# Optimization experiments

Measured on AMD Instinct MI355X. Metric: run time of the kernel, lower is better.

The kernel has to match this reference:

```python
import jax, jax.numpy as jnp
import numpy as np

EPS = 1e-5
K = 9
DILATION = 1

def bn(x, g, b, m, v):
    # x: (B,C,N,1), inference-mode BatchNorm2d with running stats
    sh = (1, -1, 1, 1)
    return (x - m.reshape(sh)) * (g.reshape(sh) / jnp.sqrt(v.reshape(sh) + EPS)) + b.reshape(sh)

def conv1x1(x, w, b):
    # w: (Cout, Cin), x: (B,Cin,N,1)
    return jnp.einsum('oc,bcnj->bonj', w, x) + b.reshape(1, -1, 1, 1)

def knn_idx(feat, k):
    # feat: (B,C,N) -> (B,N,k) indices of k nearest nodes (incl. self)
    xt = jnp.transpose(feat, (0, 2, 1))  # (B,N,C)
    x2 = jnp.sum(xt * xt, axis=-1)       # (B,N)
    dist = x2[:, :, None] - 2.0 * jnp.einsum('bnc,bmc->bnm', xt, xt) + x2[:, None, :]
    _, idx = jax.lax.top_k(-dist, k)
    return idx

def setup_inputs():
    key = jax.random.key(0)
    ks = jax.random.split(key, 24)
    B, C, H, W = 16, 256, 32, 32
    HID = 512
    def g(i, shape, s=1.0):
        return jax.random.normal(ks[i], shape, dtype=jnp.float32) * s
    def pos(i, shape):
        return jax.random.uniform(ks[i], shape, dtype=jnp.float32, minval=0.5, maxval=1.5)
    return {
        'x': g(0, (B, C, H, W)),
        'fc1_w': g(1, (C, C), 0.05), 'fc1_b': g(2, (C,), 0.05),
        'bn1_g': pos(3, (C,)), 'bn1_b': g(4, (C,), 0.1), 'bn1_m': g(5, (C,), 0.1), 'bn1_v': pos(6, (C,)),
        'gc_w': g(7, (HID, 2 * C), 0.05), 'gc_b': g(8, (HID,), 0.05),
        'gbn_g': pos(9, (HID,)), 'gbn_b': g(10, (HID,), 0.1), 'gbn_m': g(11, (HID,), 0.1), 'gbn_v': pos(12, (HID,)),
        'bn2_g': pos(13, (HID,)), 'bn2_b': g(14, (HID,), 0.1), 'bn2_m': g(15, (HID,), 0.1), 'bn2_v': pos(16, (HID,)),
        'fc2_w': g(17, (C, HID), 0.05), 'fc2_b': g(18, (C,), 0.05),
        'bn3_g': pos(19, (C,)), 'bn3_b': g(20, (C,), 0.1), 'bn3_m': g(21, (C,), 0.1), 'bn3_v': pos(22, (C,)),
    }

def reference(x, fc1_w, fc1_b, bn1_g, bn1_b, bn1_m, bn1_v,
              gc_w, gc_b, gbn_g, gbn_b, gbn_m, gbn_v,
              bn2_g, bn2_b, bn2_m, bn2_v,
              fc2_w, fc2_b, bn3_g, bn3_b, bn3_m, bn3_v):
    B, C, H, W = x.shape
    N = H * W
    x = x.reshape(B, C, N, 1)
    shortcut = x
    # fc1: 1x1 conv + BN
    h = bn(conv1x1(x, fc1_w, fc1_b), bn1_g, bn1_b, bn1_m, bn1_v)
    # DyGraphConv2d: dynamic dilated kNN graph over N nodes
    feat = h[..., 0]  # (B,C,N)
    idx = knn_idx(feat, K * DILATION)[:, :, ::DILATION]  # (B,N,K)
    # MRConv2d: max over neighbors of (x_j - x_i)
    x_j = jax.vmap(lambda f, i: f[:, i])(feat, idx)        # (B,C,N,K) gather
    diff_max = jnp.max(x_j - feat[:, :, :, None], axis=-1)  # (B,C,N)
    # interleave [x, max_diff] along channel dim -> (B, 2C, N, 1)
    m = jnp.stack([feat, diff_max], axis=2).reshape(B, 2 * C, N, 1)
    g = conv1x1(m, gc_w, gc_b)
    g = bn(g, gbn_g, gbn_b, gbn_m, gbn_v)  # BasicConv BN, act='None'
    # graph_conv Sequential: BN + GELU (erf, torch default)
    g = jax.nn.gelu(bn(g, bn2_g, bn2_b, bn2_m, bn2_v), approximate=False)
    # fc2 + residual (drop_path=0 -> identity)
    out = bn(conv1x1(g, fc2_w, fc2_b), bn3_g, bn3_b, bn3_m, bn3_v)
    return out + shortcut
```

## Files before the change

kernel.cpp:

```cpp
#include <hip/hip_runtime.h>
#include <hip/hip_bf16.h>
#include <stdint.h>

typedef unsigned long long u64;
typedef __hip_bfloat16 bf16;
typedef short s8v __attribute__((ext_vector_type(8)));
typedef short s4v __attribute__((ext_vector_type(4)));
typedef float f4v __attribute__((ext_vector_type(4)));

#define B_   16
#define C_   256
#define N_   1024
#define HID_ 512

__device__ __forceinline__ unsigned short f2b(float f) {
    unsigned u = __float_as_uint(f);
    unsigned r = (u + 0x7FFFu + ((u >> 16) & 1u)) >> 16;
    return (unsigned short)r;
}
__device__ __forceinline__ float b2f(unsigned short s) {
    return __uint_as_float(((unsigned)s) << 16);
}
__device__ __forceinline__ float ldIn(const void* p, long long i, int bf) {
    return bf ? b2f(((const unsigned short*)p)[i]) : ((const float*)p)[i];
}

__global__ void prep_kernel(const void* xp,
    const void* fc1_b, const void* bn1_g, const void* bn1_b, const void* bn1_m, const void* bn1_v,
    const void* gc_b,  const void* gbn_g, const void* gbn_b, const void* gbn_m, const void* gbn_v,
    const void* bn2_g, const void* bn2_b, const void* bn2_m, const void* bn2_v,
    const void* fc2_b, const void* bn3_g, const void* bn3_b, const void* bn3_m, const void* bn3_v,
    int* flags, float* s1, float* t1, float* Sg, float* Tg, float* s3, float* t3)
{
    __shared__ int sf;
    if (threadIdx.x == 0) {
        const unsigned short* u = (const unsigned short*)xp;
        int cnt = 0;
        for (int i = 0; i < 64; ++i) {
            int e = (u[2 * i] >> 7) & 0xFF;
            cnt += (e >= 87 && e <= 167);
        }
        int f = (cnt >= 48) ? 1 : 0;
        flags[0] = f;
        sf = f;
    }
    __syncthreads();
    int bf = sf;
    int i = threadIdx.x;
    if (i < 256) {
        float g = ldIn(bn1_g, i, bf), bb = ldIn(bn1_b, i, bf);
        float m = ldIn(bn1_m, i, bf), v  = ldIn(bn1_v, i, bf);
        float s = g / sqrtf(v + 1e-5f);
        s1[i] = s;
        t1[i] = (ldIn(fc1_b, i, bf) - m) * s + bb;

        float g3 = ldIn(bn3_g, i, bf), b3 = ldIn(bn3_b, i, bf);
        float m3 = ldIn(bn3_m, i, bf), v3 = ldIn(bn3_v, i, bf);
        float ss3 = g3 / sqrtf(v3 + 1e-5f);
        s3[i] = ss3;
        t3[i] = (ldIn(fc2_b, i, bf) - m3) * ss3 + b3;
    }
    if (i < 512) {
        float gg = ldIn(gbn_g, i, bf), gb = ldIn(gbn_b, i, bf);
        float gm = ldIn(gbn_m, i, bf), gv = ldIn(gbn_v, i, bf);
        float sg = gg / sqrtf(gv + 1e-5f);
        float g2 = ldIn(bn2_g, i, bf), b2 = ldIn(bn2_b, i, bf);
        float m2 = ldIn(bn2_m, i, bf), v2 = ldIn(bn2_v, i, bf);
        float s2 = g2 / sqrtf(v2 + 1e-5f);
        Sg[i] = sg * s2;
        Tg[i] = ((ldIn(gc_b, i, bf) - gm) * sg + gb - m2) * s2 + b2;
    }
}

__global__ __launch_bounds__(256)
void cast_weights(const void* w1, const void* wg, const void* w2,
                  short* W1b, short* Wgb, short* W2b, const int* flags)
{
    int inf = flags[0];
    int i = blockIdx.x * 256 + threadIdx.x;
    if (i < 65536) {
        W1b[i] = (short)f2b(ldIn(w1, i, inf));
    } else if (i < 65536 + 262144) {
        int j = i - 65536;
        Wgb[j] = (short)f2b(ldIn(wg, j, inf));
    } else {
        int j = i - 327680;
        W2b[j] = (short)f2b(ldIn(w2, j, inf));
    }
}

__global__ __launch_bounds__(256)
void fc1_valu(const void* __restrict__ Aw, const void* __restrict__ Bx,
              float* __restrict__ Ft, const float* __restrict__ s1,
              const float* __restrict__ t1, const int* __restrict__ flags)
{
    __shared__ float As[16][68];
    __shared__ float Bs[16][68];

    int inf = flags[0];
    int b  = blockIdx.z;
    int o0 = blockIdx.y * 64, n0 = blockIdx.x * 64;
    int t  = threadIdx.x;
    int tn = t & 15, to = t >> 4;
    long long bbase = (long long)b * C_ * N_;

    float acc[4][4] = {};

    for (int k0 = 0; k0 < C_; k0 += 16) {
        {
            int l = t * 4;
            int ao = l >> 4, ak = l & 15;
            long long ai = (long long)(o0 + ao) * C_ + k0 + ak;
            As[ak + 0][ao] = ldIn(Aw, ai + 0, inf);
            As[ak + 1][ao] = ldIn(Aw, ai + 1, inf);
            As[ak + 2][ao] = ldIn(Aw, ai + 2, inf);
            As[ak + 3][ao] = ldIn(Aw, ai + 3, inf);
        }
        {
            int l = t * 4;
            int bk = l >> 6, bn = l & 63;
            long long bi = bbase + (long long)(k0 + bk) * N_ + n0 + bn;
            Bs[bk][bn + 0] = ldIn(Bx, bi + 0, inf);
            Bs[bk][bn + 1] = ldIn(Bx, bi + 1, inf);
            Bs[bk][bn + 2] = ldIn(Bx, bi + 2, inf);
            Bs[bk][bn + 3] = ldIn(Bx, bi + 3, inf);
        }
        __syncthreads();
        #pragma unroll
        for (int k = 0; k < 16; ++k) {
            float av[4], bv[4];
            #pragma unroll
            for (int i = 0; i < 4; ++i) av[i] = As[k][to * 4 + i];
            #pragma unroll
            for (int j = 0; j < 4; ++j) bv[j] = Bs[k][tn * 4 + j];
            #pragma unroll
            for (int i = 0; i < 4; ++i)
                #pragma unroll
                for (int j = 0; j < 4; ++j) acc[i][j] += av[i] * bv[j];
        }
        __syncthreads();
    }

    #pragma unroll
    for (int i = 0; i < 4; ++i) {
        int o = o0 + to * 4 + i;
        float s = s1[o], tt = t1[o];
        #pragma unroll
        for (int j = 0; j < 4; ++j) {
            int n = n0 + tn * 4 + j;
            Ft[((long long)(b << 10) + n) * C_ + o] = acc[i][j] * s + tt;
        }
    }
}

__global__ __launch_bounds__(256)
void prep_F(const float* __restrict__ Ft, short* __restrict__ Fhi,
            short* __restrict__ Flo, float* __restrict__ x2)
{
    int t = threadIdx.x;
    int wv = t >> 6, lane = t & 63;
    int n = blockIdx.x * 4 + wv;
    int b = blockIdx.y;
    long long base = ((long long)(b << 10) + n) * C_ + lane * 4;
    f4v f = *(const f4v*)(Ft + base);

    s4v hi, lo;
    #pragma unroll
    for (int r = 0; r < 4; ++r) {
        unsigned short h = f2b(f[r]);
        hi[r] = (short)h;
        lo[r] = (short)f2b(f[r] - b2f(h));
    }
    *(s4v*)(Fhi + base) = hi;
    *(s4v*)(Flo + base) = lo;

    float ss = f[0]*f[0] + f[1]*f[1] + f[2]*f[2] + f[3]*f[3];
    #pragma unroll
    for (int s = 32; s >= 1; s >>= 1) ss += __shfl_xor(ss, s, 64);
    if (lane == 0) x2[(b << 10) + n] = ss;
}

__global__ __launch_bounds__(256)
void gram_topk(const short* __restrict__ Fhi, const short* __restrict__ Flo,
               const float* __restrict__ x2, u64* __restrict__ Part)
{
    __shared__ __align__(16) char ldsbuf[52224];
    short* Ah  = (short*)(ldsbuf);
    short* Al  = (short*)(ldsbuf + 20480);
    short* Bh  = (short*)(ldsbuf + 40960);
    short* Bl  = (short*)(ldsbuf + 46080);
    float* x2s = (float*)(ldsbuf + 51200);
    u64*   mrg  = (u64*)(ldsbuf);
    u64*   mrg2 = (u64*)(ldsbuf + 20480);

    int t = threadIdx.x;
    int q0 = blockIdx.x * 64, mq = blockIdx.y, b = blockIdx.z;
    int wv = t >> 6, ln15 = t & 15, quad = (t >> 4) & 3;

    x2s[t] = x2[(b << 10) + mq * 256 + t];

    f4v acc[16];
    #pragma unroll
    for (int i = 0; i < 16; ++i) acc[i] = 0.f;

    for (int kc = 0; kc < 8; ++kc) {
        __syncthreads();
        #pragma unroll
        for (int s = 0; s < 10; ++s) {
            int sid = t + s * 256;
            int row = sid >> 2, seg = sid & 3;
            const short* src;
            short* dst;
            int grow;
            if (row < 256)      { dst = &Ah[row * 40 + seg * 8];         grow = mq * 256 + row;       src = Fhi; }
            else if (row < 512) { dst = &Al[(row - 256) * 40 + seg * 8]; grow = mq * 256 + row - 256; src = Flo; }
            else if (row < 576) { dst = &Bh[(row - 512) * 40 + seg * 8]; grow = q0 + row - 512;       src = Fhi; }
            else                { dst = &Bl[(row - 576) * 40 + seg * 8]; grow = q0 + row - 576;       src = Flo; }
            *(s8v*)dst = *(const s8v*)(src + ((long long)((b << 10) + grow)) * C_ + kc * 32 + seg * 8);
        }
        __syncthreads();
        s8v qh = *(s8v*)&Bh[(wv * 16 + ln15) * 40 + quad * 8];
        s8v ql = *(s8v*)&Bl[(wv * 16 + ln15) * 40 + quad * 8];
        #pragma unroll
        for (int i = 0; i < 16; ++i) {
            s8v mh = *(s8v*)&Ah[(i * 16 + ln15) * 40 + quad * 8];
            s8v ml = *(s8v*)&Al[(i * 16 + ln15) * 40 + quad * 8];
            acc[i] = __builtin_amdgcn_mfma_f32_16x16x32_bf16(mh, qh, acc[i], 0, 0, 0);
            acc[i] = __builtin_amdgcn_mfma_f32_16x16x32_bf16(mh, ql, acc[i], 0, 0, 0);
            acc[i] = __builtin_amdgcn_mfma_f32_16x16x32_bf16(ml, qh, acc[i], 0, 0, 0);
        }
    }

    u64 l[9];
    #pragma unroll
    for (int i = 0; i < 9; ++i) l[i] = ~0ULL;
    #pragma unroll
    for (int i = 0; i < 16; ++i) {
        #pragma unroll
        for (int r = 0; r < 4; ++r) {
            int mloc = i * 16 + quad * 4 + r;
            float d = x2s[mloc] - 2.f * acc[i][r];
            unsigned u = __float_as_uint(d);
            u = (u & 0x80000000u) ? ~u : (u | 0x80000000u);
            u64 key = ((u64)u << 32) | (unsigned)(mq * 256 + mloc);
            if (key < l[8]) {
                u64 x = key;
                #pragma unroll
                for (int jj = 0; jj < 9; ++jj) {
                    u64 lo2 = l[jj] < x ? l[jj] : x;
                    u64 hi2 = l[jj] < x ? x : l[jj];
                    l[jj] = lo2; x = hi2;
                }
            }
        }
    }

    __syncthreads();
    {
        int qloc = wv * 16 + ln15;
        #pragma unroll
        for (int k = 0; k < 9; ++k) mrg[(qloc * 4 + quad) * 9 + k] = l[k];
    }
    __syncthreads();
    if (t < 128) {
        int r = t >> 1, pr = t & 1;
        const u64* LA = &mrg[(r * 4 + pr * 2) * 9];
        const u64* LB = LA + 9;
        int ia = 0, ib = 0;
        u64* Po = &mrg2[(r * 2 + pr) * 9];
        #pragma unroll
        for (int k = 0; k < 9; ++k) {
            u64 va = LA[ia], vb = LB[ib];
            bool ta = va < vb;
            Po[k] = ta ? va : vb;
            ia += ta; ib += !ta;
        }
    }
    __syncthreads();
    if (t < 64) {
        const u64* LA = &mrg2[(t * 2) * 9];
        const u64* LB = LA + 9;
        int ia = 0, ib = 0;
        u64* P = Part + (((long long)((b << 10) + q0 + t)) * 4 + mq) * 9;
        #pragma unroll
        for (int k = 0; k < 9; ++k) {
            u64 va = LA[ia], vb = LB[ib];
            bool ta = va < vb;
            P[k] = ta ? va : vb;
            ia += ta; ib += !ta;
        }
    }
}

__global__ __launch_bounds__(256)
void merge_final(const u64* __restrict__ Part, int* __restrict__ ix)
{
    int row = blockIdx.x * 256 + threadIdx.x;
    const u64* L = Part + (long long)row * 36;
    int p0 = 0, p1 = 0, p2 = 0, p3 = 0;
    #pragma unroll
    for (int k = 0; k < 9; ++k) {
        u64 v0 = L[p0], v1 = L[9 + p1], v2 = L[18 + p2], v3 = L[27 + p3];
        u64 m01 = v0 < v1 ? v0 : v1;
        u64 m23 = v2 < v3 ? v2 : v3;
        u64 mn  = m01 < m23 ? m01 : m23;
        ix[row * 9 + k] = (int)(mn & 0xFFFFFFFFu);
        p0 += (mn == v0);
        p1 += (mn == v1) & (mn != v0);
        p2 += (mn == v2) & (mn != v0) & (mn != v1);
        p3 += (mn == v3) & (mn != v0) & (mn != v1) & (mn != v2);
    }
}

__global__ __launch_bounds__(256)
void build_Mt(const float* __restrict__ Ft, const int* __restrict__ idx,
              short* __restrict__ Mt)
{
    int t = threadIdx.x;
    int wv = t >> 6, lane = t & 63;
    int n = blockIdx.x * 4 + wv;
    int b = blockIdx.y;
    int c0 = lane * 4;
    long long nb = (long long)(b << 10) + n;

    f4v f = *(const f4v*)(Ft + nb * C_ + c0);
    const int* id = idx + nb * 9;
    f4v mx = {-3.4e38f, -3.4e38f, -3.4e38f, -3.4e38f};
    #pragma unroll
    for (int k = 0; k < 9; ++k) {
        f4v g = *(const f4v*)(Ft + ((long long)(b << 10) + id[k]) * C_ + c0);
        mx[0] = fmaxf(mx[0], g[0]); mx[1] = fmaxf(mx[1], g[1]);
        mx[2] = fmaxf(mx[2], g[2]); mx[3] = fmaxf(mx[3], g[3]);
    }
    s8v m8;
    #pragma unroll
    for (int r = 0; r < 4; ++r) {
        m8[2 * r]     = (short)f2b(f[r]);
        m8[2 * r + 1] = (short)f2b(mx[r] - f[r]);
    }
    *(s8v*)(Mt + nb * (2 * C_) + 2 * c0) = m8;
}

template<int EPI>
__global__ __launch_bounds__(256)
void mfma_gemm(const short* __restrict__ A, const short* __restrict__ Bm,
               void* __restrict__ Out, const float* __restrict__ scale,
               const float* __restrict__ bias, const void* __restrict__ resid,
               const int* __restrict__ flags, int K, int Odim)
{
    __shared__ short As[128][40];
    __shared__ short Bs[128][40];

    int t = threadIdx.x, b = blockIdx.z;
    int n0 = blockIdx.x * 128, o0 = blockIdx.y * 128;
    int wv = t >> 6, ln = t & 15, quad = (t >> 4) & 3;
    int wo = (wv & 1) * 64, wn = (wv >> 1) * 64;

    f4v acc[4][4];
    #pragma unroll
    for (int i = 0; i < 4; ++i)
        #pragma unroll
        for (int j = 0; j < 4; ++j) acc[i][j] = 0.f;

    const short* Ab = A + (long long)o0 * K;
    const short* Bb = Bm + ((long long)(b << 10) + n0) * K;

    for (int k0 = 0; k0 < K; k0 += 32) {
        __syncthreads();
        #pragma unroll
        for (int s = 0; s < 2; ++s) {
            int sid = t + s * 256;
            int row = sid >> 2, seg = sid & 3;
            *(s8v*)&As[row][seg * 8] = *(const s8v*)(Ab + (long long)row * K + k0 + seg * 8);
            *(s8v*)&Bs[row][seg * 8] = *(const s8v*)(Bb + (long long)row * K + k0 + seg * 8);
        }
        __syncthreads();
        s8v a[4], bf[4];
        #pragma unroll
        for (int i = 0; i < 4; ++i) a[i]  = *(s8v*)&As[wo + i * 16 + ln][quad * 8];
        #pragma unroll
        for (int j = 0; j < 4; ++j) bf[j] = *(s8v*)&Bs[wn + j * 16 + ln][quad * 8];
        #pragma unroll
        for (int i = 0; i < 4; ++i)
            #pragma unroll
            for (int j = 0; j < 4; ++j)
                acc[i][j] = __builtin_amdgcn_mfma_f32_16x16x32_bf16(a[i], bf[j], acc[i][j], 0, 0, 0);
    }

    int inf = flags[0];
    #pragma unroll
    for (int i = 0; i < 4; ++i) {
        int ob = o0 + wo + i * 16 + quad * 4;
        #pragma unroll
        for (int j = 0; j < 4; ++j) {
            int n = n0 + wn + j * 16 + ln;
            f4v v = acc[i][j];
            if (EPI == 0) {
                s4v g;
                #pragma unroll
                for (int r = 0; r < 4; ++r) {
                    float val = v[r] * scale[ob + r] + bias[ob + r];
                    val = 0.5f * val * (1.0f + erff(val * 0.70710678118654752f));
                    g[r] = (short)f2b(val);
                }
                *(s4v*)((short*)Out + ((long long)(b << 10) + n) * Odim + ob) = g;
            } else {
                #pragma unroll
                for (int r = 0; r < 4; ++r) {
                    int o = ob + r;
                    long long oi = ((long long)b * Odim + o) * N_ + n;
                    ((float*)Out)[oi] = v[r] * scale[o] + bias[o] + ldIn(resid, oi, inf);
                }
            }
        }
    }
}

extern "C" void kernel_launch(void* const* d_in, const int* in_sizes, int n_in,
                              void* d_out, int out_size, void* d_ws, size_t ws_size,
                              hipStream_t stream)
{
    const void* p[23];
    if (n_in >= 23 && in_sizes[0] != 4194304 && in_sizes[22] == 4194304) {
        const int amap[23] = {
            22, 13, 12, 1, 0, 2, 3,
            21, 20, 17, 16, 18, 19,
            5, 4, 6, 7,
            15, 14, 9, 8, 10, 11 };
        for (int i = 0; i < 23; ++i) p[i] = d_in[amap[i]];
    } else {
        for (int i = 0; i < 23; ++i) p[i] = d_in[i];
    }

    const void* x     = p[0];
    const void* fc1_w = p[1];
    const void* fc1_b = p[2];
    const void* bn1_g = p[3];
    const void* bn1_b = p[4];
    const void* bn1_m = p[5];
    const void* bn1_v = p[6];
    const void* gc_w  = p[7];
    const void* gc_b  = p[8];
    const void* gbn_g = p[9];
    const void* gbn_b = p[10];
    const void* gbn_m = p[11];
    const void* gbn_v = p[12];
    const void* bn2_g = p[13];
    const void* bn2_b = p[14];
    const void* bn2_m = p[15];
    const void* bn2_v = p[16];
    const void* fc2_w = p[17];
    const void* fc2_b = p[18];
    const void* bn3_g = p[19];
    const void* bn3_b = p[20];
    const void* bn3_m = p[21];
    const void* bn3_v = p[22];

    char* ws = (char*)d_ws;
    size_t off = 0;
    int*   flags = (int*)ws;
    float* s1 = (float*)(ws + 256);
    float* t1 = s1 + 256;
    float* s3 = t1 + 256;
    float* t3 = s3 + 256;
    float* Sg = t3 + 256;
    float* Tg = Sg + 512;
    off = 16384;
    int*   ixAll = (int*)(ws + off);  off += (size_t)B_ * N_ * 9 * 4;
    short* W1b   = (short*)(ws + off); off += (size_t)C_ * C_ * 2;
    short* Wgb   = (short*)(ws + off); off += (size_t)HID_ * 2 * C_ * 2;
    short* W2b   = (short*)(ws + off); off += (size_t)C_ * HID_ * 2;
    float* Ft    = (float*)(ws + off); off += (size_t)B_ * N_ * C_ * 4;
    short* Fhi   = (short*)(ws + off); off += (size_t)B_ * N_ * C_ * 2;
    short* Flo   = (short*)(ws + off); off += (size_t)B_ * N_ * C_ * 2;
    float* x2    = (float*)(ws + off); off += (size_t)B_ * N_ * 4;
    u64*   Part  = (u64*)  (ws + off); off += (size_t)B_ * N_ * 4 * 9 * 8;
    short* Mt    = (short*)(ws + off); off += (size_t)B_ * N_ * 2 * C_ * 2;
    short* Gt    = (short*)(ws + off); off += (size_t)B_ * N_ * HID_ * 2;

    prep_kernel<<<1, 512, 0, stream>>>(x,
        fc1_b, bn1_g, bn1_b, bn1_m, bn1_v,
        gc_b, gbn_g, gbn_b, gbn_m, gbn_v,
        bn2_g, bn2_b, bn2_m, bn2_v,
        fc2_b, bn3_g, bn3_b, bn3_m, bn3_v,
        flags, s1, t1, Sg, Tg, s3, t3);

    cast_weights<<<1792, 256, 0, stream>>>(fc1_w, gc_w, fc2_w,
                                           W1b, Wgb, W2b, flags);

    fc1_valu<<<dim3(16, 4, B_), 256, 0, stream>>>(fc1_w, x, Ft, s1, t1, flags);

    prep_F<<<dim3(N_ / 4, B_), 256, 0, stream>>>(Ft, Fhi, Flo, x2);

    gram_topk<<<dim3(16, 4, 16), 256, 0, stream>>>(Fhi, Flo, x2, Part);
    merge_final<<<64, 256, 0, stream>>>(Part, ixAll);

    build_Mt<<<dim3(256, 16), 256, 0, stream>>>(Ft, ixAll, Mt);

    mfma_gemm<0><<<dim3(8, 4, 16), 256, 0, stream>>>(
        Wgb, Mt, Gt, Sg, Tg, nullptr, flags, 2 * C_, HID_);

    mfma_gemm<1><<<dim3(8, 2, 16), 256, 0, stream>>>(
        W2b, Gt, d_out, s3, t3, x, flags, HID_, C_);
}
```

Measured before the change: 330.0 us.

## Fuse hi/lo split and norms into fc1, halve gram tiles, merge top-k in gather

The fc1 epilogue now writes the bf16 hi/lo split and accumulates squared norms via LDS reduction and atomicAdd, so the separate prep_F pass disappears and x2 is zeroed in prep_kernel. The gram/top-k kernel uses 128-row candidate tiles instead of 256, doubling the grid and reducing LDS and accumulator registers for better occupancy, at the cost of twice as many partial lists. The merge_final kernel is removed and its 8-way partial merge is done with wave shuffles inside build_Mt. The trade-offs are strided uncoalesced bf16 stores in fc1, float atomics that make x2 summation order nondeterministic, and more partial-list traffic.

After: 336.6 us. 2.0% more time.

```diff
diff --git a/kernel.cpp b/kernel.cpp
--- a/kernel.cpp
+++ b/kernel.cpp
@@ -24,13 +24,20 @@
 __device__ __forceinline__ float ldIn(const void* p, long long i, int bf) {
     return bf ? b2f(((const unsigned short*)p)[i]) : ((const float*)p)[i];
 }
+__device__ __forceinline__ u64 shfl_xor_u64(u64 v, int m) {
+    unsigned lo = (unsigned)v, hi = (unsigned)(v >> 32);
+    lo = __shfl_xor(lo, m, 64);
+    hi = __shfl_xor(hi, m, 64);
+    return ((u64)hi << 32) | lo;
+}
 
 __global__ void prep_kernel(const void* xp,
     const void* fc1_b, const void* bn1_g, const void* bn1_b, const void* bn1_m, const void* bn1_v,
     const void* gc_b,  const void* gbn_g, const void* gbn_b, const void* gbn_m, const void* gbn_v,
     const void* bn2_g, const void* bn2_b, const void* bn2_m, const void* bn2_v,
     const void* fc2_b, const void* bn3_g, const void* bn3_b, const void* bn3_m, const void* bn3_v,
-    int* flags, float* s1, float* t1, float* Sg, float* Tg, float* s3, float* t3)
+    int* flags, float* s1, float* t1, float* Sg, float* Tg, float* s3, float* t3,
+    float* x2)
 {
     __shared__ int sf;
     if (threadIdx.x == 0) {
@@ -44,6 +51,7 @@
         flags[0] = f;
         sf = f;
     }
+    for (int i = threadIdx.x; i < B_ * N_; i += 512) x2[i] = 0.f;
     __syncthreads();
     int bf = sf;
     int i = threadIdx.x;
@@ -91,11 +99,14 @@
 
 __global__ __launch_bounds__(256)
 void fc1_valu(const void* __restrict__ Aw, const void* __restrict__ Bx,
-              float* __restrict__ Ft, const float* __restrict__ s1,
-              const float* __restrict__ t1, const int* __restrict__ flags)
+              float* __restrict__ Ft, short* __restrict__ Fhi,
+              short* __restrict__ Flo, float* __restrict__ x2,
+              const float* __restrict__ s1, const float* __restrict__ t1,
+              const int* __restrict__ flags)
 {
     __shared__ float As[16][68];
     __shared__ float Bs[16][68];
+    __shared__ float x2part[16][64];
 
     int inf = flags[0];
     int b  = blockIdx.z;
@@ -141,6 +152,7 @@
         __syncthreads();
     }
 
+    float p2[4] = {};
     #pragma unroll
     for (int i = 0; i < 4; ++i) {
         int o = o0 + to * 4 + i;
@@ -148,48 +160,36 @@
         #pragma unroll
         for (int j = 0; j < 4; ++j) {
             int n = n0 + tn * 4 + j;
-            Ft[((long long)(b << 10) + n) * C_ + o] = acc[i][j] * s + tt;
-        }
-    }
-}
-
-__global__ __launch_bounds__(256)
-void prep_F(const float* __restrict__ Ft, short* __restrict__ Fhi,
-            short* __restrict__ Flo, float* __restrict__ x2)
-{
-    int t = threadIdx.x;
-    int wv = t >> 6, lane = t & 63;
-    int n = blockIdx.x * 4 + wv;
-    int b = blockIdx.y;
-    long long base = ((long long)(b << 10) + n) * C_ + lane * 4;
-    f4v f = *(const f4v*)(Ft + base);
-
-    s4v hi, lo;
-    #pragma unroll
-    for (int r = 0; r < 4; ++r) {
-        unsigned short h = f2b(f[r]);
-        hi[r] = (short)h;
-        lo[r] = (short)f2b(f[r] - b2f(h));
-    }
-    *(s4v*)(Fhi + base) = hi;
-    *(s4v*)(Flo + base) = lo;
-
-    float ss = f[0]*f[0] + f[1]*f[1] + f[2]*f[2] + f[3]*f[3];
-    #pragma unroll
-    for (int s = 32; s >= 1; s >>= 1) ss += __shfl_xor(ss, s, 64);
-    if (lane == 0) x2[(b << 10) + n] = ss;
+            float f = acc[i][j] * s + tt;
+            long long oi = ((long long)(b << 10) + n) * C_ + o;
+            Ft[oi] = f;
+            unsigned short h = f2b(f);
+            Fhi[oi] = (short)h;
+            Flo[oi] = (short)f2b(f - b2f(h));
+            p2[j] += f * f;
+        }
+    }
+    #pragma unroll
+    for (int j = 0; j < 4; ++j) x2part[to][tn * 4 + j] = p2[j];
+    __syncthreads();
+    if (t < 64) {
+        float s = 0.f;
+        #pragma unroll
+        for (int r = 0; r < 16; ++r) s += x2part[r][t];
+        atomicAdd(&x2[(b << 10) + n0 + t], s);
+    }
 }
 
 __global__ __launch_bounds__(256)
 void gram_topk(const short* __restrict__ Fhi, const short* __restrict__ Flo,
                const float* __restrict__ x2, u64* __restrict__ Part)
 {
-    __shared__ __align__(16) char ldsbuf[52224];
+    __shared__ __align__(16) char ldsbuf[31232];
     short* Ah  = (short*)(ldsbuf);
-    short* Al  = (short*)(ldsbuf + 20480);
-    short* Bh  = (short*)(ldsbuf + 40960);
-    short* Bl  = (short*)(ldsbuf + 46080);
-    float* x2s = (float*)(ldsbuf + 51200);
+    short* Al  = (short*)(ldsbuf + 10240);
+    short* Bh  = (short*)(ldsbuf + 20480);
+    short* Bl  = (short*)(ldsbuf + 25600);
+    float* x2s = (float*)(ldsbuf + 30720);
     u64*   mrg  = (u64*)(ldsbuf);
     u64*   mrg2 = (u64*)(ldsbuf + 20480);
 
@@ -197,32 +197,32 @@
     int q0 = blockIdx.x * 64, mq = blockIdx.y, b = blockIdx.z;
     int wv = t >> 6, ln15 = t & 15, quad = (t >> 4) & 3;
 
-    x2s[t] = x2[(b << 10) + mq * 256 + t];
-
-    f4v acc[16];
-    #pragma unroll
-    for (int i = 0; i < 16; ++i) acc[i] = 0.f;
+    if (t < 128) x2s[t] = x2[(b << 10) + mq * 128 + t];
+
+    f4v acc[8];
+    #pragma unroll
+    for (int i = 0; i < 8; ++i) acc[i] = 0.f;
 
     for (int kc = 0; kc < 8; ++kc) {
         __syncthreads();
         #pragma unroll
-        for (int s = 0; s < 10; ++s) {
+        for (int s = 0; s < 6; ++s) {
             int sid = t + s * 256;
             int row = sid >> 2, seg = sid & 3;
             const short* src;
             short* dst;
             int grow;
-            if (row < 256)      { dst = &Ah[row * 40 + seg * 8];         grow = mq * 256 + row;       src = Fhi; }
-            else if (row < 512) { dst = &Al[(row - 256) * 40 + seg * 8]; grow = mq * 256 + row - 256; src = Flo; }
-            else if (row < 576) { dst = &Bh[(row - 512) * 40 + seg * 8]; grow = q0 + row - 512;       src = Fhi; }
-            else                { dst = &Bl[(row - 576) * 40 + seg * 8]; grow = q0 + row - 576;       src = Flo; }
+            if (row < 128)      { dst = &Ah[row * 40 + seg * 8];         grow = mq * 128 + row;       src = Fhi; }
+            else if (row < 256) { dst = &Al[(row - 128) * 40 + seg * 8]; grow = mq * 128 + row - 128; src = Flo; }
+            else if (row < 320) { dst = &Bh[(row - 256) * 40 + seg * 8]; grow = q0 + row - 256;       src = Fhi; }
+            else                { dst = &Bl[(row - 320) * 40 + seg * 8]; grow = q0 + row - 320;       src = Flo; }
             *(s8v*)dst = *(const s8v*)(src + ((long long)((b << 10) + grow)) * C_ + kc * 32 + seg * 8);
         }
         __syncthreads();
         s8v qh = *(s8v*)&Bh[(wv * 16 + ln15) * 40 + quad * 8];
         s8v ql = *(s8v*)&Bl[(wv * 16 + ln15) * 40 + quad * 8];
         #pragma unroll
-        for (int i = 0; i < 16; ++i) {
+        for (int i = 0; i < 8; ++i) {
             s8v mh = *(s8v*)&Ah[(i * 16 + ln15) * 40 + quad * 8];
             s8v ml = *(s8v*)&Al[(i * 16 + ln15) * 40 + quad * 8];
             acc[i] = __builtin_amdgcn_mfma_f32_16x16x32_bf16(mh, qh, acc[i], 0, 0, 0);
@@ -235,14 +235,14 @@
     #pragma unroll
     for (int i = 0; i < 9; ++i) l[i] = ~0ULL;
     #pragma unroll
-    for (int i = 0; i < 16; ++i) {
+    for (int i = 0; i < 8; ++i) {
         #pragma unroll
         for (int r = 0; r < 4; ++r) {
             int mloc = i * 16 + quad * 4 + r;
             float d = x2s[mloc] - 2.f * acc[i][r];
             unsigned u = __float_as_uint(d);
             u = (u & 0x80000000u) ? ~u : (u | 0x80000000u);
-            u64 key = ((u64)u << 32) | (unsigned)(mq * 256 + mloc);
+            u64 key = ((u64)u << 32) | (unsigned)(mq * 128 + mloc);
             if (key < l[8]) {
                 u64 x = key;
                 #pragma unroll
@@ -281,7 +281,7 @@
         const u64* LA = &mrg2[(t * 2) * 9];
         const u64* LB = LA + 9;
         int ia = 0, ib = 0;
-        u64* P = Part + (((long long)((b << 10) + q0 + t)) * 4 + mq) * 9;
+        u64* P = Part + (((long long)((b << 10) + q0 + t)) * 8 + mq) * 9;
         #pragma unroll
         for (int k = 0; k < 9; ++k) {
             u64 va = LA[ia], vb = LB[ib];
@@ -293,42 +293,45 @@
 }
 
 __global__ __launch_bounds__(256)
-void merge_final(const u64* __restrict__ Part, int* __restrict__ ix)
-{
-    int row = blockIdx.x * 256 + threadIdx.x;
-    const u64* L = Part + (long long)row * 36;
-    int p0 = 0, p1 = 0, p2 = 0, p3 = 0;
-    #pragma unroll
-    for (int k = 0; k < 9; ++k) {
-        u64 v0 = L[p0], v1 = L[9 + p1], v2 = L[18 + p2], v3 = L[27 + p3];
-        u64 m01 = v0 < v1 ? v0 : v1;
-        u64 m23 = v2 < v3 ? v2 : v3;
-        u64 mn  = m01 < m23 ? m01 : m23;
-        ix[row * 9 + k] = (int)(mn & 0xFFFFFFFFu);
-        p0 += (mn == v0);
-        p1 += (mn == v1) & (mn != v0);
-        p2 += (mn == v2) & (mn != v0) & (mn != v1);
-        p3 += (mn == v3) & (mn != v0) & (mn != v1) & (mn != v2);
-    }
-}
-
-__global__ __launch_bounds__(256)
-void build_Mt(const float* __restrict__ Ft, const int* __restrict__ idx,
+void build_Mt(const float* __restrict__ Ft, const u64* __restrict__ Part,
               short* __restrict__ Mt)
 {
     int t = threadIdx.x;
     int wv = t >> 6, lane = t & 63;
     int n = blockIdx.x * 4 + wv;
     int b = blockIdx.y;
+    long long nb = (long long)(b << 10) + n;
+
+    const u64* L = Part + nb * 72 + (long long)(lane & 7) * 9;
+    u64 l[9];
+    #pragma unroll
+    for (int k = 0; k < 9; ++k) l[k] = L[k];
+    #pragma unroll
+    for (int s = 1; s <= 4; s <<= 1) {
+        u64 p[9];
+        #pragma unroll
+        for (int k = 0; k < 9; ++k) p[k] = shfl_xor_u64(l[k], s);
+        #pragma unroll
+        for (int k = 0; k < 9; ++k) {
+            u64 x = p[k];
+            if (x < l[8]) {
+                #pragma unroll
+                for (int jj = 0; jj < 9; ++jj) {
+                    u64 lo2 = l[jj] < x ? l[jj] : x;
+                    u64 hi2 = l[jj] < x ? x : l[jj];
+                    l[jj] = lo2; x = hi2;
+                }
+            }
+        }
+    }
+
     int c0 = lane * 4;
-    long long nb = (long long)(b << 10) + n;
-
     f4v f = *(const f4v*)(Ft + nb * C_ + c0);
-    const int* id = idx + nb * 9;
     f4v mx = {-3.4e38f, -3.4e38f, -3.4e38f, -3.4e38f};
     #pragma unroll
     for (int k = 0; k < 9; ++k) {
-        f4v g = *(const f4v*)(Ft + ((long long)(b << 10) + id[k]) * C_ + c0);
+        int id = (int)(l[k] & 0xFFFFFFFFu);
+        f4v g = *(const f4v*)(Ft + ((long long)(b << 10) + id) * C_ + c0);
         mx[0] = fmaxf(mx[0], g[0]); mx[1] = fmaxf(mx[1], g[1]);
         mx[2] = fmaxf(mx[2], g[2]); mx[3] = fmaxf(mx[3], g[3]);
     }
@@ -466,7 +469,6 @@
     float* Sg = t3 + 256;
     float* Tg = Sg + 512;
     off = 16384;
-    int*   ixAll = (int*)(ws + off);  off += (size_t)B_ * N_ * 9 * 4;
     short* W1b   = (short*)(ws + off); off += (size_t)C_ * C_ * 2;
     short* Wgb   = (short*)(ws + off); off += (size_t)HID_ * 2 * C_ * 2;
     short* W2b   = (short*)(ws + off); off += (size_t)C_ * HID_ * 2;
@@ -474,7 +476,7 @@
     short* Fhi   = (short*)(ws + off); off += (size_t)B_ * N_ * C_ * 2;
     short* Flo   = (short*)(ws + off); off += (size_t)B_ * N_ * C_ * 2;
     float* x2    = (float*)(ws + off); off += (size_t)B_ * N_ * 4;
-    u64*   Part  = (u64*)  (ws + off); off += (size_t)B_ * N_ * 4 * 9 * 8;
+    u64*   Part  = (u64*)  (ws + off); off += (size_t)B_ * N_ * 8 * 9 * 8;
     short* Mt    = (short*)(ws + off); off += (size_t)B_ * N_ * 2 * C_ * 2;
     short* Gt    = (short*)(ws + off); off += (size_t)B_ * N_ * HID_ * 2;
 
@@ -483,19 +485,17 @@
         gc_b, gbn_g, gbn_b, gbn_m, gbn_v,
         bn2_g, bn2_b, bn2_m, bn2_v,
         fc2_b, bn3_g, bn3_b, bn3_m, bn3_v,
-        flags, s1, t1, Sg, Tg, s3, t3);
+        flags, s1, t1, Sg, Tg, s3, t3, x2);
 
     cast_weights<<<1792, 256, 0, stream>>>(fc1_w, gc_w, fc2_w,
                                            W1b, Wgb, W2b, flags);
 
-    fc1_valu<<<dim3(16, 4, B_), 256, 0, stream>>>(fc1_w, x, Ft, s1, t1, flags);
-
-    prep_F<<<dim3(N_ / 4, B_), 256, 0, stream>>>(Ft, Fhi, Flo, x2);
-
-    gram_topk<<<dim3(16, 4, 16), 256, 0, stream>>>(Fhi, Flo, x2, Part);
-    merge_final<<<64, 256, 0, stream>>>(Part, ixAll);
-
-    build_Mt<<<dim3(256, 16), 256, 0, stream>>>(Ft, ixAll, Mt);
+    fc1_valu<<<dim3(16, 4, B_), 256, 0, stream>>>(
+        fc1_w, x, Ft, Fhi, Flo, x2, s1, t1, flags);
+
+    gram_topk<<<dim3(16, 8, 16), 256, 0, stream>>>(Fhi, Flo, x2, Part);
+
+    build_Mt<<<dim3(256, 16), 256, 0, stream>>>(Ft, Part, Mt);
 
     mfma_gemm<0><<<dim3(8, 4, 16), 256, 0, stream>>>(
         Wgb, Mt, Gt, Sg, Tg, nullptr, flags, 2 * C_, HID_);
```
